# Optimization experiments

Measured on AMD Instinct MI355X. Metric: run time of the kernel, lower is better.

Reference implementation:

```python
import jax, jax.numpy as jnp
import numpy as np

N = 200000      # total nodes
B = 1024        # graphs
D = 256         # node_dim
OUT = 256       # out_dim


def setup_inputs() -> dict:
    key = jax.random.key(0)
    ks = jax.random.split(key, 16)
    x = jax.random.normal(ks[0], (N, D), dtype=jnp.float32)
    # sorted segment ids covering all B graphs (no empty segments)
    extra = jax.random.randint(ks[1], (N - B,), 0, B)
    batch = jnp.sort(jnp.concatenate([jnp.arange(B, dtype=jnp.int32), extra.astype(jnp.int32)]))
    # one-hot node type mask [N, 3]
    types = jax.random.randint(ks[2], (N,), 0, 3)
    node_type_mask = jax.nn.one_hot(types, 3, dtype=jnp.int32)
    s = 1.0 / np.sqrt(D)
    # attn_weight: Linear(D, D//2) -> Tanh -> Linear(D//2, 1)
    aw1 = jax.random.uniform(ks[3], (D, D // 2), jnp.float32, -s, s)
    ab1 = jnp.zeros((D // 2,), jnp.float32)
    aw2 = jax.random.uniform(ks[4], (D // 2, 1), jnp.float32, -s, s)
    ab2 = jnp.zeros((1,), jnp.float32)
    # three typed transforms Linear(D, D)
    we = jax.random.uniform(ks[5], (D, D), jnp.float32, -s, s)
    be = jnp.zeros((D,), jnp.float32)
    wv = jax.random.uniform(ks[6], (D, D), jnp.float32, -s, s)
    bv = jnp.zeros((D,), jnp.float32)
    wp = jax.random.uniform(ks[7], (D, D), jnp.float32, -s, s)
    bp = jnp.zeros((D,), jnp.float32)
    # readout MLP: Linear(3D, 2*OUT) -> SiLU -> (Dropout eval) -> Linear(2*OUT, OUT)
    w1 = jax.random.uniform(ks[8], (3 * D, 2 * OUT), jnp.float32, -1.0 / np.sqrt(3 * D), 1.0 / np.sqrt(3 * D))
    b1 = jnp.zeros((2 * OUT,), jnp.float32)
    w2 = jax.random.uniform(ks[9], (2 * OUT, OUT), jnp.float32, -1.0 / np.sqrt(2 * OUT), 1.0 / np.sqrt(2 * OUT))
    b2 = jnp.zeros((OUT,), jnp.float32)
    return dict(x=x, batch=batch, node_type_mask=node_type_mask, num_segments=B,
                aw1=aw1, ab1=ab1, aw2=aw2, ab2=ab2, we=we, be=be, wv=wv, bv=bv,
                wp=wp, bp=bp, w1=w1, b1=b1, w2=w2, b2=b2)


def reference(x, batch, node_type_mask, num_segments,
              aw1, ab1, aw2, ab2, we, be, wv, bv, wp, bp, w1, b1, w2, b2):
    nseg = int(num_segments)
    # global_mean_pool
    counts = jax.ops.segment_sum(jnp.ones((x.shape[0],), x.dtype), batch, num_segments=nseg)
    mean_pool = jax.ops.segment_sum(x, batch, num_segments=nseg) / counts[:, None]
    # attention scores + segment softmax
    scores = jnp.tanh(x @ aw1 + ab1) @ aw2 + ab2            # [N, 1]
    s = scores[:, 0]
    m = jax.ops.segment_max(s, batch, num_segments=nseg)    # [B]
    e = jnp.exp(s - m[batch])
    z = jax.ops.segment_sum(e, batch, num_segments=nseg)
    attn = e / z[batch]                                     # [N]
    attn_pool = jax.ops.segment_sum(x * attn[:, None], batch, num_segments=nseg)
    # typed physical pooling (node_type_mask path)
    mask = node_type_mask.astype(x.dtype)
    typed_x = (mask[:, 0:1] * (x @ we + be)
               + mask[:, 1:2] * (x @ wv + bv)
               + mask[:, 2:3] * (x @ wp + bp))
    phys_pool = jax.ops.segment_sum(typed_x, batch, num_segments=nseg)
    combined = jnp.concatenate([mean_pool, attn_pool, phys_pool], axis=-1)  # [B, 3D]
    h = jax.nn.silu(combined @ w1 + b1)                     # dropout = identity (eval)
    return h @ w2 + b2                                      # [B, OUT]
```

## Files before the change

### kernel.cpp

```cpp
#include <hip/hip_runtime.h>

typedef float  f32x4  __attribute__((ext_vector_type(4)));
typedef short  s16x8  __attribute__((ext_vector_type(8)));
typedef short  s16x4  __attribute__((ext_vector_type(4)));

__device__ __forceinline__ short f2bf(float f) {
  unsigned u = __float_as_uint(f);
  u += 0x7fffu + ((u >> 16) & 1u);
  return (short)(u >> 16);
}
__device__ __forceinline__ float bf2f(unsigned short us) {
  return __uint_as_float(((unsigned)us) << 16);
}
__device__ __forceinline__ float tanh_fast(float x) {
  const float e = __expf(2.0f * x);
  return 1.0f - 2.0f / (e + 1.0f);
}

__global__ __launch_bounds__(256) void k_cvtw(
    const float* __restrict__ aw1, const float* __restrict__ we, const float* __restrict__ wv,
    const float* __restrict__ wp, const float* __restrict__ w1, const float* __restrict__ w2,
    unsigned short* __restrict__ Awt, unsigned short* __restrict__ Wpt,
    unsigned short* __restrict__ W1t, unsigned short* __restrict__ W2t,
    float* __restrict__ Z) {
  const int b = blockIdx.x, tid = threadIdx.x;
  if (b >= 184) {
    const int idx = b - 184;
    f32x4* Z4 = reinterpret_cast<f32x4*>(Z);
    const f32x4 z4 = {0.f, 0.f, 0.f, 0.f};
#pragma unroll
    for (int j = 0; j < 4; ++j) {
      const int o = idx * 1024 + j * 256 + tid;
      if (o < 263168) Z4[o] = z4;
    }
    return;
  }
  __shared__ short T[64][65];
  const float* src; unsigned short* dst;
  int N, ds, off, t;
  if (b < 8)        { src = aw1; dst = Awt; N = 128; ds = 256; off = 0;   t = b; }
  else if (b < 24)  { src = we;  dst = Wpt; N = 256; ds = 768; off = 0;   t = b - 8; }
  else if (b < 40)  { src = wv;  dst = Wpt; N = 256; ds = 768; off = 256; t = b - 24; }
  else if (b < 56)  { src = wp;  dst = Wpt; N = 256; ds = 768; off = 512; t = b - 40; }
  else if (b < 152) { src = w1;  dst = W1t; N = 512; ds = 768; off = 0;   t = b - 56; }
  else              { src = w2;  dst = W2t; N = 256; ds = 512; off = 0;   t = b - 152; }
  const int ntx = N >> 6;
  const int kt = t / ntx;
  const int k0 = kt * 64, n0 = (t - kt * ntx) * 64;
  const int rl = tid >> 6, cl = tid & 63;
#pragma unroll
  for (int i = 0; i < 16; ++i)
    T[cl][i * 4 + rl] = f2bf(src[(size_t)(k0 + i * 4 + rl) * N + n0 + cl]);
  __syncthreads();
#pragma unroll
  for (int i = 0; i < 16; ++i)
    dst[(size_t)(n0 + i * 4 + rl) * ds + off + k0 + cl] = (unsigned short)T[i * 4 + rl][cl];
}

__global__ __launch_bounds__(256, 2) void k_score_pool(
    const float* __restrict__ x, const int* __restrict__ batch, const int* __restrict__ mask,
    const unsigned short* __restrict__ Awt, const float* __restrict__ ab1,
    const float* __restrict__ aw2, const float* __restrict__ ab2,
    float* __restrict__ P, float* __restrict__ EX, float* __restrict__ ZC,
    int nnodes) {
  __shared__ __align__(16) short xs[32][264];
  __shared__ __align__(16) short xsB[8192];
  __shared__ __align__(16) float sred[4][32];
  __shared__ __align__(16) short em[16][40];
  __shared__ int st_all[320];

  const int tid  = threadIdx.x;
  const int lane = tid & 63;
  const int w    = tid >> 6;
  const int quad = lane >> 4;
  const int l15  = lane & 15;

  s16x8 bfrag[8][2];
  float ab1v[2], aw2v[2];
#pragma unroll
  for (int ct = 0; ct < 2; ++ct) {
    const int col = w * 32 + ct * 16 + l15;
    ab1v[ct] = ab1[col];
    aw2v[ct] = aw2[col];
    const s16x8* bp = reinterpret_cast<const s16x8*>(Awt + (size_t)col * 256);
#pragma unroll
    for (int kt = 0; kt < 8; ++kt) bfrag[kt][ct] = bp[kt * 4 + quad];
  }
  const float ab2v = ab2[0];

  const int tiles = nnodes >> 5;
  const int t_beg = (int)(((long long)blockIdx.x * tiles) / (long long)gridDim.x);
  const int t_end = (int)(((long long)(blockIdx.x + 1) * tiles) / (long long)gridDim.x);
  if (t_beg >= t_end) return;

  {
    const int nodes0 = t_beg * 32, nblk = (t_end - t_beg) * 32;
    for (int i = tid; i < nblk; i += 256) {
      const int g = nodes0 + i;
      st_all[i] = batch[g] * 4 + mask[g * 3 + 1] + 2 * mask[g * 3 + 2];
    }
    for (int i = tid; i < 640; i += 256) (&em[0][0])[i] = 0;
  }

  f32x4 stg[8];
  auto load_regs = [&](int tile) {
    const f32x4* xp = reinterpret_cast<const f32x4*>(x + (size_t)tile * 8192);
#pragma unroll
    for (int i = 0; i < 8; ++i) stg[i] = xp[(8 * w + i) * 64 + lane];
  };
  auto cvt_write = [&]() {
    s16x4 xv[8];
#pragma unroll
    for (int i = 0; i < 8; ++i) {
      xv[i][0] = f2bf(stg[i][0]); xv[i][1] = f2bf(stg[i][1]);
      xv[i][2] = f2bf(stg[i][2]); xv[i][3] = f2bf(stg[i][3]);
    }
#pragma unroll
    for (int i = 0; i < 8; ++i)
      *reinterpret_cast<s16x4*>(&xs[8 * w + i][lane * 4]) = xv[i];
    const int gb = (lane >> 2) * 4 + w;
    const int lb = (lane & 3) * 4;
#pragma unroll
    for (int q = 0; q < 4; ++q) {
      s16x8 v;
#pragma unroll
      for (int j = 0; j < 8; ++j) v[j] = xv[j][q];
      *reinterpret_cast<s16x8*>(&xsB[(gb * 16 + lb + q) * 8]) = v;
    }
  };

  load_regs(t_beg);
  cvt_write();
  __syncthreads();

  const f32x4 zero4 = {0.f, 0.f, 0.f, 0.f};
  f32x4 accB[4] = {zero4, zero4, zero4, zero4};
  float zA = 0.f, c0A = 0.f, c1A = 0.f, c2A = 0.f;
  int cur = -1;

  auto flushB = [&]() {
#pragma unroll
    for (int c = 0; c < 4; ++c) {
      const int col = w * 64 + c * 16 + l15;
      if (quad == 0) {
        atomicAdd(&EX[cur * 256 + col], accB[c][0] + accB[c][1]);
        atomicAdd(&P[cur * 768 + col], accB[c][2]);
        atomicAdd(&P[cur * 768 + 256 + col], accB[c][3]);
      } else if (quad == 1) {
        atomicAdd(&P[cur * 768 + 512 + col], accB[c][0]);
      }
      accB[c] = zero4;
    }
    if (w == 0) {
      if (lane < 4) {
        const float v = (lane == 0) ? zA : ((lane == 1) ? c0A : ((lane == 2) ? c1A : c2A));
        atomicAdd(&ZC[cur * 4 + lane], v);
      }
      zA = c0A = c1A = c2A = 0.f;
    }
  };

  for (int tile = t_beg; tile < t_end; ++tile) {
    const bool more = (tile + 1 < t_end);
    if (more) load_regs(tile + 1);

#pragma unroll
    for (int ng = 0; ng < 2; ++ng) {
      s16x8 af[8];
#pragma unroll
      for (int kt = 0; kt < 8; ++kt)
        af[kt] = *reinterpret_cast<const s16x8*>(&xs[16 * ng + l15][kt * 32 + quad * 8]);
      float part[4] = {0.f, 0.f, 0.f, 0.f};
#pragma unroll
      for (int ct = 0; ct < 2; ++ct) {
        f32x4 acc = {0.f, 0.f, 0.f, 0.f};
#pragma unroll
        for (int kt = 0; kt < 8; ++kt)
          acc = __builtin_amdgcn_mfma_f32_16x16x32_bf16(af[kt], bfrag[kt][ct], acc, 0, 0, 0);
#pragma unroll
        for (int r = 0; r < 4; ++r)
          part[r] += tanh_fast(acc[r] + ab1v[ct]) * aw2v[ct];
      }
#pragma unroll
      for (int off = 1; off < 16; off <<= 1) {
#pragma unroll
        for (int r = 0; r < 4; ++r) part[r] += __shfl_xor(part[r], off);
      }
      if (l15 == 0) {
#pragma unroll
        for (int r = 0; r < 4; ++r) sred[w][16 * ng + quad * 4 + r] = part[r];
      }
    }

    s16x8 bfB[4];
#pragma unroll
    for (int c = 0; c < 4; ++c)
      bfB[c] = *reinterpret_cast<const s16x8*>(
          &xsB[(((w * 4 + c) * 4 + quad) * 16 + l15) * 8]);

    __syncthreads();

    const int base = (tile - t_beg) * 32;

    float e_f = 0.f;
    int myt = 3;
    if (lane < 32) {
      const float s = ab2v + sred[0][lane] + sred[1][lane] + sred[2][lane] + sred[3][lane];
      e_f = __expf(s);
      const unsigned short hi = (unsigned short)f2bf(e_f);
      const unsigned short lo = (unsigned short)f2bf(e_f - bf2f(hi));
      myt = st_all[base + lane] & 3;
      em[0][lane] = (short)hi;
      em[1][lane] = (short)lo;
      em[2][lane] = (myt == 0) ? (short)0x3f80 : (short)0;
      em[3][lane] = (myt == 1) ? (short)0x3f80 : (short)0;
      em[4][lane] = (myt == 2) ? (short)0x3f80 : (short)0;
    }
    const int myseg = (lane < 32) ? (st_all[base + lane] >> 2) : 0x7fffffff;

    s16x8 emf = *reinterpret_cast<const s16x8*>(&em[l15][quad * 8]);

    int n0 = 0;
    while (n0 < 32) {
      const int seg = st_all[base + n0] >> 2;
      const unsigned long long diff = __ballot(lane < 32 && myseg != seg) >> n0;
      const int n1 = (diff == 0) ? 32 : n0 + (int)__builtin_ctzll(diff);
      if (seg != cur) { if (cur >= 0) flushB(); cur = seg; }
      s16x8 af;
      const int kb = quad * 8;
#pragma unroll
      for (int j = 0; j < 8; ++j) {
        const int k = kb + j;
        af[j] = (k >= n0 && k < n1) ? emf[j] : (short)0;
      }
#pragma unroll
      for (int c = 0; c < 4; ++c)
        accB[c] = __builtin_amdgcn_mfma_f32_16x16x32_bf16(af, bfB[c], accB[c], 0, 0, 0);
      if (w == 0) {
        const bool inrun = (lane >= n0 && lane < n1 && lane < 32);
        float ee = inrun ? e_f : 0.f;
#pragma unroll
        for (int off = 1; off < 32; off <<= 1) ee += __shfl_xor(ee, off);
        const unsigned long long b0 = __ballot(inrun && myt == 0);
        const unsigned long long b1 = __ballot(inrun && myt == 1);
        const unsigned long long b2 = __ballot(inrun && myt == 2);
        zA  += ee;
        c0A += (float)__popcll(b0);
        c1A += (float)__popcll(b1);
        c2A += (float)__popcll(b2);
      }
      n0 = n1;
    }

    if (more) cvt_write();
    __syncthreads();
  }
  if (cur >= 0) flushB();
}

__global__ __launch_bounds__(256) void k_phys(
    const float* __restrict__ P, const unsigned short* __restrict__ Wpt,
    const float* __restrict__ be, const float* __restrict__ bv, const float* __restrict__ bp,
    const float* __restrict__ ZC, float* __restrict__ PH) {
  __shared__ __align__(16) short as16[16][776];
  const int tid = threadIdx.x, lane = tid & 63, w = tid >> 6;
  const int quad = lane >> 4, l15 = lane & 15;
  const int rowbase = blockIdx.x * 16;
  const int col = blockIdx.y * 64 + w * 16 + l15;

  s16x8 bfr[24];
  const s16x8* bpf = reinterpret_cast<const s16x8*>(Wpt + (size_t)col * 768);
#pragma unroll
  for (int kt = 0; kt < 24; ++kt) bfr[kt] = bpf[kt * 4 + quad];

  const f32x4* ap = reinterpret_cast<const f32x4*>(P + (size_t)rowbase * 768);
#pragma unroll
  for (int i = 0; i < 12; ++i) {
    const int ci = tid + 256 * i;
    f32x4 v = ap[ci];
    const int row = ci / 192, c4 = (ci % 192) * 4;
    s16x4 b; b[0] = f2bf(v[0]); b[1] = f2bf(v[1]); b[2] = f2bf(v[2]); b[3] = f2bf(v[3]);
    *reinterpret_cast<s16x4*>(&as16[row][c4]) = b;
  }
  __syncthreads();

  f32x4 acc = {0.f, 0.f, 0.f, 0.f};
#pragma unroll
  for (int kt = 0; kt < 24; ++kt) {
    s16x8 af = *reinterpret_cast<const s16x8*>(&as16[l15][kt * 32 + quad * 8]);
    acc = __builtin_amdgcn_mfma_f32_16x16x32_bf16(af, bfr[kt], acc, 0, 0, 0);
  }
  const float ben = be[col], bvn = bv[col], bpn = bp[col];
#pragma unroll
  for (int r = 0; r < 4; ++r) {
    const int row = rowbase + quad * 4 + r;
    const float v = acc[r] + ZC[row * 4 + 1] * ben + ZC[row * 4 + 2] * bvn + ZC[row * 4 + 3] * bpn;
    PH[(size_t)row * 256 + col] = v;
  }
}

__global__ __launch_bounds__(256) void k_mlp1(
    const float* __restrict__ P, const float* __restrict__ EX,
    const float* __restrict__ ZC, const float* __restrict__ PH,
    const unsigned short* __restrict__ W1t, const float* __restrict__ b1,
    float* __restrict__ H) {
  __shared__ __align__(16) short as16[16][776];
  const int tid = threadIdx.x, lane = tid & 63, w = tid >> 6;
  const int quad = lane >> 4, l15 = lane & 15;
  const int rowbase = blockIdx.x * 16;
  const int col = blockIdx.y * 64 + w * 16 + l15;

  s16x8 bfr[24];
  const s16x8* bpf = reinterpret_cast<const s16x8*>(W1t + (size_t)col * 768);
#pragma unroll
  for (int kt = 0; kt < 24; ++kt) bfr[kt] = bpf[kt * 4 + quad];

#pragma unroll 4
  for (int r = 0; r < 16; ++r) {
    const int row = rowbase + r;
    const float z   = ZC[row * 4 + 0];
    const float cnt = ZC[row * 4 + 1] + ZC[row * 4 + 2] + ZC[row * 4 + 3];
    const float mp  = (P[(size_t)row * 768 + tid] + P[(size_t)row * 768 + 256 + tid] +
                       P[(size_t)row * 768 + 512 + tid]) / cnt;
    as16[r][tid]       = f2bf(mp);
    as16[r][256 + tid] = f2bf(EX[(size_t)row * 256 + tid] / z);
    as16[r][512 + tid] = f2bf(PH[(size_t)row * 256 + tid]);
  }
  __syncthreads();

  f32x4 acc = {0.f, 0.f, 0.f, 0.f};
#pragma unroll
  for (int kt = 0; kt < 24; ++kt) {
    s16x8 af = *reinterpret_cast<const s16x8*>(&as16[l15][kt * 32 + quad * 8]);
    acc = __builtin_amdgcn_mfma_f32_16x16x32_bf16(af, bfr[kt], acc, 0, 0, 0);
  }
  const float bn = b1[col];
#pragma unroll
  for (int r = 0; r < 4; ++r) {
    const int row = rowbase + quad * 4 + r;
    const float v = acc[r] + bn;
    H[(size_t)row * 512 + col] = v / (1.f + __expf(-v));
  }
}

__global__ __launch_bounds__(256) void k_mlp2(
    const float* __restrict__ A, const unsigned short* __restrict__ W2t,
    const float* __restrict__ b2, float* __restrict__ out) {
  __shared__ __align__(16) short as16[16][520];
  const int tid = threadIdx.x, lane = tid & 63, w = tid >> 6;
  const int quad = lane >> 4, l15 = lane & 15;
  const int rowbase = blockIdx.x * 16;
  const int col = blockIdx.y * 64 + w * 16 + l15;

  s16x8 bfr[16];
  const s16x8* bpf = reinterpret_cast<const s16x8*>(W2t + (size_t)col * 512);
#pragma unroll
  for (int kt = 0; kt < 16; ++kt) bfr[kt] = bpf[kt * 4 + quad];

  const f32x4* ap = reinterpret_cast<const f32x4*>(A + (size_t)rowbase * 512);
#pragma unroll
  for (int i = 0; i < 8; ++i) {
    const int ci = tid + 256 * i;
    f32x4 v = ap[ci];
    const int row = ci >> 7, c4 = (ci & 127) * 4;
    s16x4 b; b[0] = f2bf(v[0]); b[1] = f2bf(v[1]); b[2] = f2bf(v[2]); b[3] = f2bf(v[3]);
    *reinterpret_cast<s16x4*>(&as16[row][c4]) = b;
  }
  __syncthreads();

  f32x4 acc = {0.f, 0.f, 0.f, 0.f};
#pragma unroll
  for (int kt = 0; kt < 16; ++kt) {
    s16x8 af = *reinterpret_cast<const s16x8*>(&as16[l15][kt * 32 + quad * 8]);
    acc = __builtin_amdgcn_mfma_f32_16x16x32_bf16(af, bfr[kt], acc, 0, 0, 0);
  }
  const float bn = b2[col];
#pragma unroll
  for (int r = 0; r < 4; ++r) {
    const int row = rowbase + quad * 4 + r;
    out[(size_t)row * 256 + col] = acc[r] + bn;
  }
}

extern "C" void kernel_launch(void* const* d_in, const int* in_sizes, int n_in,
                              void* d_out, int out_size, void* d_ws, size_t ws_size,
                              hipStream_t stream) {
  const float* x    = (const float*)d_in[0];
  const int*   batch= (const int*)  d_in[1];
  const int*   mask = (const int*)  d_in[2];
  const float* aw1  = (const float*)d_in[4];
  const float* ab1  = (const float*)d_in[5];
  const float* aw2  = (const float*)d_in[6];
  const float* ab2  = (const float*)d_in[7];
  const float* we   = (const float*)d_in[8];
  const float* be   = (const float*)d_in[9];
  const float* wv   = (const float*)d_in[10];
  const float* bv   = (const float*)d_in[11];
  const float* wp   = (const float*)d_in[12];
  const float* bp   = (const float*)d_in[13];
  const float* w1   = (const float*)d_in[14];
  const float* b1   = (const float*)d_in[15];
  const float* w2   = (const float*)d_in[16];
  const float* b2   = (const float*)d_in[17];
  float* out = (float*)d_out;
  const int nn = in_sizes[1];

  float* ws = (float*)d_ws;
  float* P    = ws;
  float* EXs  = P    + 786432;
  float* ZCs  = EXs  + 262144;
  float* PH   = ZCs  + 4096;
  float* hbuf = PH   + 262144;
  unsigned short* Awt = (unsigned short*)(hbuf + 524288);
  unsigned short* Wpt = Awt + 32768;
  unsigned short* W1t = Wpt + 196608;
  unsigned short* W2t = W1t + 393216;

  k_cvtw      <<<456, 256, 0, stream>>>(aw1, we, wv, wp, w1, w2, Awt, Wpt, W1t, W2t, P);
  k_score_pool<<<1024, 256, 0, stream>>>(x, batch, mask, Awt, ab1, aw2, ab2, P, EXs, ZCs, nn);
  k_phys      <<<dim3(64, 4), 256, 0, stream>>>(P, Wpt, be, bv, bp, ZCs, PH);
  k_mlp1      <<<dim3(64, 8), 256, 0, stream>>>(P, EXs, ZCs, PH, W1t, b1, hbuf);
  k_mlp2      <<<dim3(64, 4), 256, 0, stream>>>(hbuf, W2t, b2, out);
}
```

Before: 349.3 us.

## Software-pipeline score and pooling stages with double-buffered LDS tiles

Double-buffers the bf16 x tile, its transposed copy and the per-wave score partials in LDS. The segment-pooling MFMA pass for the previous tile now runs in the same iteration as the attention-score MFMA pass for the current tile. This cuts the per-tile barriers from two to one and lets the two stages interleave. The cost is roughly double the LDS footprint, which may limit how many blocks fit on a CU, plus extra registers to carry the B fragments across iterations.

```diff
diff --git a/kernel.cpp b/kernel.cpp
--- a/kernel.cpp
+++ b/kernel.cpp
@@ -63,9 +63,9 @@
     const float* __restrict__ aw2, const float* __restrict__ ab2,
     float* __restrict__ P, float* __restrict__ EX, float* __restrict__ ZC,
     int nnodes) {
-  __shared__ __align__(16) short xs[32][264];
-  __shared__ __align__(16) short xsB[8192];
-  __shared__ __align__(16) float sred[4][32];
+  __shared__ __align__(16) short xs[2][32][264];
+  __shared__ __align__(16) short xsB[2][8192];
+  __shared__ __align__(16) float sred[2][4][32];
   __shared__ __align__(16) short em[16][40];
   __shared__ int st_all[320];
 
@@ -92,9 +92,10 @@
   const int t_beg = (int)(((long long)blockIdx.x * tiles) / (long long)gridDim.x);
   const int t_end = (int)(((long long)(blockIdx.x + 1) * tiles) / (long long)gridDim.x);
   if (t_beg >= t_end) return;
+  const int nt = t_end - t_beg;
 
   {
-    const int nodes0 = t_beg * 32, nblk = (t_end - t_beg) * 32;
+    const int nodes0 = t_beg * 32, nblk = nt * 32;
     for (int i = tid; i < nblk; i += 256) {
       const int g = nodes0 + i;
       st_all[i] = batch[g] * 4 + mask[g * 3 + 1] + 2 * mask[g * 3 + 2];
@@ -108,7 +109,7 @@
 #pragma unroll
     for (int i = 0; i < 8; ++i) stg[i] = xp[(8 * w + i) * 64 + lane];
   };
-  auto cvt_write = [&]() {
+  auto cvt_write = [&](int bb) {
     s16x4 xv[8];
 #pragma unroll
     for (int i = 0; i < 8; ++i) {
@@ -117,7 +118,7 @@
     }
 #pragma unroll
     for (int i = 0; i < 8; ++i)
-      *reinterpret_cast<s16x4*>(&xs[8 * w + i][lane * 4]) = xv[i];
+      *reinterpret_cast<s16x4*>(&xs[bb][8 * w + i][lane * 4]) = xv[i];
     const int gb = (lane >> 2) * 4 + w;
     const int lb = (lane & 3) * 4;
 #pragma unroll
@@ -125,18 +126,19 @@
       s16x8 v;
 #pragma unroll
       for (int j = 0; j < 8; ++j) v[j] = xv[j][q];
-      *reinterpret_cast<s16x8*>(&xsB[(gb * 16 + lb + q) * 8]) = v;
+      *reinterpret_cast<s16x8*>(&xsB[bb][(gb * 16 + lb + q) * 8]) = v;
     }
   };
 
   load_regs(t_beg);
-  cvt_write();
+  cvt_write(0);
   __syncthreads();
 
   const f32x4 zero4 = {0.f, 0.f, 0.f, 0.f};
   f32x4 accB[4] = {zero4, zero4, zero4, zero4};
   float zA = 0.f, c0A = 0.f, c1A = 0.f, c2A = 0.f;
   int cur = -1;
+  s16x8 bfBp[4];
 
   auto flushB = [&]() {
 #pragma unroll
@@ -160,52 +162,13 @@
     }
   };
 
-  for (int tile = t_beg; tile < t_end; ++tile) {
-    const bool more = (tile + 1 < t_end);
-    if (more) load_regs(tile + 1);
-
-#pragma unroll
-    for (int ng = 0; ng < 2; ++ng) {
-      s16x8 af[8];
-#pragma unroll
-      for (int kt = 0; kt < 8; ++kt)
-        af[kt] = *reinterpret_cast<const s16x8*>(&xs[16 * ng + l15][kt * 32 + quad * 8]);
-      float part[4] = {0.f, 0.f, 0.f, 0.f};
-#pragma unroll
-      for (int ct = 0; ct < 2; ++ct) {
-        f32x4 acc = {0.f, 0.f, 0.f, 0.f};
-#pragma unroll
-        for (int kt = 0; kt < 8; ++kt)
-          acc = __builtin_amdgcn_mfma_f32_16x16x32_bf16(af[kt], bfrag[kt][ct], acc, 0, 0, 0);
-#pragma unroll
-        for (int r = 0; r < 4; ++r)
-          part[r] += tanh_fast(acc[r] + ab1v[ct]) * aw2v[ct];
-      }
-#pragma unroll
-      for (int off = 1; off < 16; off <<= 1) {
-#pragma unroll
-        for (int r = 0; r < 4; ++r) part[r] += __shfl_xor(part[r], off);
-      }
-      if (l15 == 0) {
-#pragma unroll
-        for (int r = 0; r < 4; ++r) sred[w][16 * ng + quad * 4 + r] = part[r];
-      }
-    }
-
-    s16x8 bfB[4];
-#pragma unroll
-    for (int c = 0; c < 4; ++c)
-      bfB[c] = *reinterpret_cast<const s16x8*>(
-          &xsB[(((w * 4 + c) * 4 + quad) * 16 + l15) * 8]);
-
-    __syncthreads();
-
-    const int base = (tile - t_beg) * 32;
-
+  auto POOL = [&](int lt_idx, int par, const s16x8* fr) {
+    const int base = lt_idx * 32;
     float e_f = 0.f;
     int myt = 3;
     if (lane < 32) {
-      const float s = ab2v + sred[0][lane] + sred[1][lane] + sred[2][lane] + sred[3][lane];
+      const float s = ab2v + sred[par][0][lane] + sred[par][1][lane] +
+                      sred[par][2][lane] + sred[par][3][lane];
       e_f = __expf(s);
       const unsigned short hi = (unsigned short)f2bf(e_f);
       const unsigned short lo = (unsigned short)f2bf(e_f - bf2f(hi));
@@ -217,7 +180,6 @@
       em[4][lane] = (myt == 2) ? (short)0x3f80 : (short)0;
     }
     const int myseg = (lane < 32) ? (st_all[base + lane] >> 2) : 0x7fffffff;
-
     s16x8 emf = *reinterpret_cast<const s16x8*>(&em[l15][quad * 8]);
 
     int n0 = 0;
@@ -235,7 +197,7 @@
       }
 #pragma unroll
       for (int c = 0; c < 4; ++c)
-        accB[c] = __builtin_amdgcn_mfma_f32_16x16x32_bf16(af, bfB[c], accB[c], 0, 0, 0);
+        accB[c] = __builtin_amdgcn_mfma_f32_16x16x32_bf16(af, fr[c], accB[c], 0, 0, 0);
       if (w == 0) {
         const bool inrun = (lane >= n0 && lane < n1 && lane < 32);
         float ee = inrun ? e_f : 0.f;
@@ -251,10 +213,58 @@
       }
       n0 = n1;
     }
-
-    if (more) cvt_write();
+  };
+
+  for (int lt = 0; lt < nt; ++lt) {
+    const int p    = lt & 1;
+    const int tile = t_beg + lt;
+    const bool more = (lt + 1 < nt);
+    if (more) load_regs(tile + 1);
+
+#pragma unroll
+    for (int ng = 0; ng < 2; ++ng) {
+      s16x8 af[8];
+#pragma unroll
+      for (int kt = 0; kt < 8; ++kt)
+        af[kt] = *reinterpret_cast<const s16x8*>(&xs[p][16 * ng + l15][kt * 32 + quad * 8]);
+      float part[4] = {0.f, 0.f, 0.f, 0.f};
+#pragma unroll
+      for (int ct = 0; ct < 2; ++ct) {
+        f32x4 acc = {0.f, 0.f, 0.f, 0.f};
+#pragma unroll
+        for (int kt = 0; kt < 8; ++kt)
+          acc = __builtin_amdgcn_mfma_f32_16x16x32_bf16(af[kt], bfrag[kt][ct], acc, 0, 0, 0);
+#pragma unroll
+        for (int r = 0; r < 4; ++r)
+          part[r] += tanh_fast(acc[r] + ab1v[ct]) * aw2v[ct];
+      }
+#pragma unroll
+      for (int off = 1; off < 16; off <<= 1) {
+#pragma unroll
+        for (int r = 0; r < 4; ++r) part[r] += __shfl_xor(part[r], off);
+      }
+      if (l15 == 0) {
+#pragma unroll
+        for (int r = 0; r < 4; ++r) sred[p][w][16 * ng + quad * 4 + r] = part[r];
+      }
+    }
+
+    s16x8 bfBn[4];
+#pragma unroll
+    for (int c = 0; c < 4; ++c)
+      bfBn[c] = *reinterpret_cast<const s16x8*>(
+          &xsB[p][(((w * 4 + c) * 4 + quad) * 16 + l15) * 8]);
+
+    if (lt > 0) POOL(lt - 1, p ^ 1, bfBp);
+
+    if (more) cvt_write(p ^ 1);
+
     __syncthreads();
-  }
+#pragma unroll
+    for (int c = 0; c < 4; ++c) bfBp[c] = bfBn[c];
+  }
+
+  POOL(nt - 1, (nt - 1) & 1, bfBp);
   if (cur >= 0) flushB();
 }
 
```

Result: slower. 428.5 us (+22.6%).

## Fuse typed physical projection into first readout MLP kernel

Applied to the files above, without the earlier changes.

Removes the separate k_phys launch and its PH global buffer by computing the typed projection of pooled per-type sums inside k_mlp1, writing it straight into shared memory as the third input segment. Each of the 8 column blocks recomputes the full 256-wide phys projection for its 16 rows, which is redundant work (8x the phys MFMAs and Wpt loads) traded for one fewer launch and a global round trip. Shared memory per block roughly doubles.

```diff
diff --git a/kernel.cpp b/kernel.cpp
--- a/kernel.cpp
+++ b/kernel.cpp
@@ -258,20 +258,19 @@
   if (cur >= 0) flushB();
 }
 
-__global__ __launch_bounds__(256) void k_phys(
-    const float* __restrict__ P, const unsigned short* __restrict__ Wpt,
-    const float* __restrict__ be, const float* __restrict__ bv, const float* __restrict__ bp,
-    const float* __restrict__ ZC, float* __restrict__ PH) {
-  __shared__ __align__(16) short as16[16][776];
+__global__ __launch_bounds__(256) void k_mlp1(
+    const float* __restrict__ P, const float* __restrict__ EX,
+    const float* __restrict__ ZC,
+    const unsigned short* __restrict__ Wpt, const float* __restrict__ be,
+    const float* __restrict__ bv, const float* __restrict__ bp,
+    const unsigned short* __restrict__ W1t, const float* __restrict__ b1,
+    float* __restrict__ H) {
+  __shared__ __align__(16) short asP[16][776];
+  __shared__ __align__(16) short asC[16][776];
   const int tid = threadIdx.x, lane = tid & 63, w = tid >> 6;
   const int quad = lane >> 4, l15 = lane & 15;
   const int rowbase = blockIdx.x * 16;
-  const int col = blockIdx.y * 64 + w * 16 + l15;
-
-  s16x8 bfr[24];
-  const s16x8* bpf = reinterpret_cast<const s16x8*>(Wpt + (size_t)col * 768);
-#pragma unroll
-  for (int kt = 0; kt < 24; ++kt) bfr[kt] = bpf[kt * 4 + quad];
+  const int col1 = blockIdx.y * 64 + w * 16 + l15;
 
   const f32x4* ap = reinterpret_cast<const f32x4*>(P + (size_t)rowbase * 768);
 #pragma unroll
@@ -280,40 +279,8 @@
     f32x4 v = ap[ci];
     const int row = ci / 192, c4 = (ci % 192) * 4;
     s16x4 b; b[0] = f2bf(v[0]); b[1] = f2bf(v[1]); b[2] = f2bf(v[2]); b[3] = f2bf(v[3]);
-    *reinterpret_cast<s16x4*>(&as16[row][c4]) = b;
-  }
-  __syncthreads();
-
-  f32x4 acc = {0.f, 0.f, 0.f, 0.f};
-#pragma unroll
-  for (int kt = 0; kt < 24; ++kt) {
-    s16x8 af = *reinterpret_cast<const s16x8*>(&as16[l15][kt * 32 + quad * 8]);
-    acc = __builtin_amdgcn_mfma_f32_16x16x32_bf16(af, bfr[kt], acc, 0, 0, 0);
-  }
-  const float ben = be[col], bvn = bv[col], bpn = bp[col];
-#pragma unroll
-  for (int r = 0; r < 4; ++r) {
-    const int row = rowbase + quad * 4 + r;
-    const float v = acc[r] + ZC[row * 4 + 1] * ben + ZC[row * 4 + 2] * bvn + ZC[row * 4 + 3] * bpn;
-    PH[(size_t)row * 256 + col] = v;
-  }
-}
-
-__global__ __launch_bounds__(256) void k_mlp1(
-    const float* __restrict__ P, const float* __restrict__ EX,
-    const float* __restrict__ ZC, const float* __restrict__ PH,
-    const unsigned short* __restrict__ W1t, const float* __restrict__ b1,
-    float* __restrict__ H) {
-  __shared__ __align__(16) short as16[16][776];
-  const int tid = threadIdx.x, lane = tid & 63, w = tid >> 6;
-  const int quad = lane >> 4, l15 = lane & 15;
-  const int rowbase = blockIdx.x * 16;
-  const int col = blockIdx.y * 64 + w * 16 + l15;
-
-  s16x8 bfr[24];
-  const s16x8* bpf = reinterpret_cast<const s16x8*>(W1t + (size_t)col * 768);
-#pragma unroll
-  for (int kt = 0; kt < 24; ++kt) bfr[kt] = bpf[kt * 4 + quad];
+    *reinterpret_cast<s16x4*>(&asP[row][c4]) = b;
+  }
 
 #pragma unroll 4
   for (int r = 0; r < 16; ++r) {
@@ -322,24 +289,52 @@
     const float cnt = ZC[row * 4 + 1] + ZC[row * 4 + 2] + ZC[row * 4 + 3];
     const float mp  = (P[(size_t)row * 768 + tid] + P[(size_t)row * 768 + 256 + tid] +
                        P[(size_t)row * 768 + 512 + tid]) / cnt;
-    as16[r][tid]       = f2bf(mp);
-    as16[r][256 + tid] = f2bf(EX[(size_t)row * 256 + tid] / z);
-    as16[r][512 + tid] = f2bf(PH[(size_t)row * 256 + tid]);
+    asC[r][tid]       = f2bf(mp);
+    asC[r][256 + tid] = f2bf(EX[(size_t)row * 256 + tid] / z);
   }
   __syncthreads();
 
+#pragma unroll 1
+  for (int c = 0; c < 4; ++c) {
+    const int pcol = w * 64 + c * 16 + l15;
+    s16x8 pb[24];
+    const s16x8* pbf = reinterpret_cast<const s16x8*>(Wpt + (size_t)pcol * 768);
+#pragma unroll
+    for (int kt = 0; kt < 24; ++kt) pb[kt] = pbf[kt * 4 + quad];
+    f32x4 acc = {0.f, 0.f, 0.f, 0.f};
+#pragma unroll
+    for (int kt = 0; kt < 24; ++kt) {
+      s16x8 af = *reinterpret_cast<const s16x8*>(&asP[l15][kt * 32 + quad * 8]);
+      acc = __builtin_amdgcn_mfma_f32_16x16x32_bf16(af, pb[kt], acc, 0, 0, 0);
+    }
+    const float ben = be[pcol], bvn = bv[pcol], bpn = bp[pcol];
+#pragma unroll
+    for (int r = 0; r < 4; ++r) {
+      const int rl = quad * 4 + r, row = rowbase + rl;
+      const float v = acc[r] + ZC[row * 4 + 1] * ben + ZC[row * 4 + 2] * bvn +
+                      ZC[row * 4 + 3] * bpn;
+      asC[rl][512 + pcol] = f2bf(v);
+    }
+  }
+
+  s16x8 bfr[24];
+  const s16x8* bpf = reinterpret_cast<const s16x8*>(W1t + (size_t)col1 * 768);
+#pragma unroll
+  for (int kt = 0; kt < 24; ++kt) bfr[kt] = bpf[kt * 4 + quad];
+  __syncthreads();
+
   f32x4 acc = {0.f, 0.f, 0.f, 0.f};
 #pragma unroll
   for (int kt = 0; kt < 24; ++kt) {
-    s16x8 af = *reinterpret_cast<const s16x8*>(&as16[l15][kt * 32 + quad * 8]);
+    s16x8 af = *reinterpret_cast<const s16x8*>(&asC[l15][kt * 32 + quad * 8]);
     acc = __builtin_amdgcn_mfma_f32_16x16x32_bf16(af, bfr[kt], acc, 0, 0, 0);
   }
-  const float bn = b1[col];
+  const float bn = b1[col1];
 #pragma unroll
   for (int r = 0; r < 4; ++r) {
     const int row = rowbase + quad * 4 + r;
     const float v = acc[r] + bn;
-    H[(size_t)row * 512 + col] = v / (1.f + __expf(-v));
+    H[(size_t)row * 512 + col1] = v / (1.f + __expf(-v));
   }
 }
 
@@ -409,8 +404,7 @@
   float* P    = ws;
   float* EXs  = P    + 786432;
   float* ZCs  = EXs  + 262144;
-  float* PH   = ZCs  + 4096;
-  float* hbuf = PH   + 262144;
+  float* hbuf = ZCs  + 4096;
   unsigned short* Awt = (unsigned short*)(hbuf + 524288);
   unsigned short* Wpt = Awt + 32768;
   unsigned short* W1t = Wpt + 196608;
@@ -418,7 +412,6 @@
 
   k_cvtw      <<<456, 256, 0, stream>>>(aw1, we, wv, wp, w1, w2, Awt, Wpt, W1t, W2t, P);
   k_score_pool<<<1024, 256, 0, stream>>>(x, batch, mask, Awt, ab1, aw2, ab2, P, EXs, ZCs, nn);
-  k_phys      <<<dim3(64, 4), 256, 0, stream>>>(P, Wpt, be, bv, bp, ZCs, PH);
-  k_mlp1      <<<dim3(64, 8), 256, 0, stream>>>(P, EXs, ZCs, PH, W1t, b1, hbuf);
+  k_mlp1      <<<dim3(64, 8), 256, 0, stream>>>(P, EXs, ZCs, Wpt, be, bv, bp, W1t, b1, hbuf);
   k_mlp2      <<<dim3(64, 4), 256, 0, stream>>>(hbuf, W2t, b2, out);
 }
```

Measured after the change: 364.4 us. +4.3%, slower.
